# Performance work log

Measured on AMD Instinct MI355X. Metric: run time of the kernel, lower is better.

The kernel has to match this reference:

```python
import jax, jax.numpy as jnp
import numpy as np

B, S, D, H = 2, 2048, 1024, 16
DK = D // H
MAX_REL = 2047          # clip range for relative distances
REL_DIM = 64            # rel_embedding dim, summed over


def setup_inputs() -> dict:
    key = jax.random.key(0)
    ks = jax.random.split(key, 12)
    sc = 1.0 / np.sqrt(D)
    inp = {
        "q": jax.random.normal(ks[0], (B, S, D), jnp.float32),
        "k": jax.random.normal(ks[1], (B, S, D), jnp.float32),
        "v": jax.random.normal(ks[2], (B, S, D), jnp.float32),
        "Wq": jax.random.normal(ks[3], (D, D), jnp.float32) * sc,
        "bq": jnp.zeros((D,), jnp.float32),
        "Wk": jax.random.normal(ks[4], (D, D), jnp.float32) * sc,
        "bk": jnp.zeros((D,), jnp.float32),
        "Wv": jax.random.normal(ks[5], (D, D), jnp.float32) * sc,
        "bv": jnp.zeros((D,), jnp.float32),
        "Wo": jax.random.normal(ks[6], (D, D), jnp.float32) * sc,
        "bo": jnp.zeros((D,), jnp.float32),
        "rel_table": jax.random.normal(ks[7], (2 * MAX_REL + 1, REL_DIM), jnp.float32) * 0.02,
        "mask": jnp.tril(jnp.ones((1, 1, S, S), jnp.bool_)),  # causal
    }
    return inp


def reference(q, k, v, Wq, bq, Wk, bk, Wv, bv, Wo, bo, rel_table, mask):
    def split_heads(x):
        # [B,S,D] -> [B,H,S,DK]
        return x.reshape(B, -1, H, DK).transpose(0, 2, 1, 3)

    Q = split_heads(q @ Wq + bq)
    K = split_heads(k @ Wk + bk)
    V = split_heads(v @ Wv + bv)

    scores = jnp.einsum("bhqd,bhkd->bhqk", Q, K) / jnp.sqrt(jnp.float32(DK))

    # relative position bias: table[clip(j - i)] summed over rel dim -> [S,S]
    rel_idx = jnp.clip(jnp.arange(S)[None, :] - jnp.arange(S)[:, None],
                       -MAX_REL, MAX_REL) + MAX_REL
    rel_bias = rel_table[rel_idx].sum(-1)  # [S,S]
    scores = scores + rel_bias[None, None]

    scores = jnp.where(mask, scores, jnp.float32(-1e20))
    attn = jax.nn.softmax(scores, axis=-1)

    out = jnp.einsum("bhqk,bhkd->bhqd", attn, V)
    out = out.transpose(0, 2, 1, 3).reshape(B, -1, D)
    return out @ Wo + bo
```

## Files before the change

kernel.cpp:

```cpp
#include <hip/hip_runtime.h>

#define SEQ 2048
#define DIM 1024
#define NH 16
#define HD 64
#define NB 2

typedef __bf16 bf16x8 __attribute__((ext_vector_type(8)));
typedef float f32x4 __attribute__((ext_vector_type(4)));
typedef float f32x4v __attribute__((ext_vector_type(4)));
typedef float f32x4u __attribute__((ext_vector_type(4), aligned(4)));
typedef unsigned short us8 __attribute__((ext_vector_type(8)));
typedef unsigned short us4 __attribute__((ext_vector_type(4)));

#define LOG2E 1.44269504f

__device__ __forceinline__ unsigned short bfbits(float f) {
  __bf16 h = (__bf16)f;
  return __builtin_bit_cast(unsigned short, h);
}

__global__ __launch_bounds__(256) void wconv4_kernel(
    const float* __restrict__ W0, const float* __restrict__ W1,
    const float* __restrict__ W2, const float* __restrict__ W3,
    unsigned short* __restrict__ Wt, const float* __restrict__ rel_table,
    float* __restrict__ relsum, const float* __restrict__ Aq,
    const float* __restrict__ Ak, const float* __restrict__ Av,
    unsigned short* __restrict__ Bq, unsigned short* __restrict__ Bk,
    unsigned short* __restrict__ Bv) {
  int z = blockIdx.z;
  int tid = threadIdx.x;
  if (z == 4) {
    int ti = blockIdx.y * 16 + blockIdx.x;
    int i = ti * 256 + tid;
    if (i < 4095) {
      const f32x4v* row = reinterpret_cast<const f32x4v*>(rel_table + (size_t)i * 64);
      float s = 0.f;
      for (int d = 0; d < 16; ++d) {
        f32x4v v = row[d];
        s += v[0] + v[1] + v[2] + v[3];
      }
      relsum[i] = s * LOG2E - 8.0f;
    }
    return;
  }
  if (z >= 5) {
    const float* src = (z == 5) ? Aq : (z == 6) ? Ak : Av;
    unsigned short* dst = (z == 5) ? Bq : (z == 6) ? Bk : Bv;
    int bid2 = blockIdx.y * 16 + blockIdx.x;
    int c0 = bid2 * 256 + tid;
    for (int j = 0; j < 8; ++j) {
      size_t e = ((size_t)(c0 + j * 65536)) * 8;
      f32x4v v0 = *reinterpret_cast<const f32x4v*>(src + e);
      f32x4v v1 = *reinterpret_cast<const f32x4v*>(src + e + 4);
      us8 o;
      o[0] = bfbits(v0[0]); o[1] = bfbits(v0[1]); o[2] = bfbits(v0[2]); o[3] = bfbits(v0[3]);
      o[4] = bfbits(v1[0]); o[5] = bfbits(v1[1]); o[6] = bfbits(v1[2]); o[7] = bfbits(v1[3]);
      *reinterpret_cast<us8*>(dst + e) = o;
    }
    return;
  }
  __shared__ unsigned short T[64][68];
  const float* W = (z == 0) ? W0 : (z == 1) ? W1 : (z == 2) ? W2 : W3;
  unsigned short* out = Wt + (size_t)z * 1024 * 1024;
  int r0 = blockIdx.y * 64;
  int c0 = blockIdx.x * 64;
  for (int it = 0; it < 4; ++it) {
    int s = tid + it * 256;
    int r = s >> 4;
    int c4 = (s & 15) * 4;
    f32x4v v = *reinterpret_cast<const f32x4v*>(W + (size_t)(r0 + r) * 1024 + c0 + c4);
    us4 o;
    o[0] = bfbits(v[0]); o[1] = bfbits(v[1]); o[2] = bfbits(v[2]); o[3] = bfbits(v[3]);
    *reinterpret_cast<us4*>(&T[r][c4]) = o;
  }
  __syncthreads();
  for (int it = 0; it < 2; ++it) {
    int s = tid + it * 256;
    int n = s >> 3;
    int k8 = (s & 7) * 8;
    us8 o;
    for (int e = 0; e < 8; ++e) o[e] = T[k8 + e][n];
    *reinterpret_cast<us8*>(out + (size_t)(c0 + n) * 1024 + r0 + k8) = o;
  }
}

__global__ __launch_bounds__(256) void gemm_qkv_kernel(
    const unsigned short* __restrict__ Aq, const unsigned short* __restrict__ Ak,
    const unsigned short* __restrict__ Av, const unsigned short* __restrict__ WTb,
    const float* __restrict__ bq, const float* __restrict__ bk,
    const float* __restrict__ bv, unsigned short* __restrict__ Qb,
    unsigned short* __restrict__ Kb, unsigned short* __restrict__ Vt,
    float qscale) {
  constexpr int N = 1024, K = 1024;
  int o = (blockIdx.x & 7) * 192 + (blockIdx.x >> 3);
  int z = o >> 9;
  int r2 = o & 511;
  int row0 = (r2 >> 4) * 128;
  int col0 = (r2 & 15) * 64;
  const unsigned short* A = (z == 0) ? Aq : (z == 1) ? Ak : Av;
  const unsigned short* WT = WTb + (size_t)z * N * K;
  const float* bias = (z == 0) ? bq : (z == 1) ? bk : bv;
  float oscale = (z == 0) ? qscale : 1.0f;

  int tid = threadIdx.x;
  int w = tid >> 6;
  int lane = tid & 63;
  int lg = lane >> 4;
  int li = lane & 15;
  int wr = (w >> 1) * 64;
  int wc = (w & 1) * 32;

  __shared__ unsigned short As[2][128][72];
  __shared__ unsigned short Ws[2][64][72];

  us8 ab16[4];
  us8 wreg[2];

#define GLOAD(KS)                                                         \
  {                                                                       \
    int k0 = (KS) * 64;                                                   \
    for (int it = 0; it < 4; ++it) {                                      \
      int s = tid + it * 256;                                             \
      int r = s >> 3;                                                     \
      int cg = (s & 7) * 8;                                               \
      ab16[it] = *reinterpret_cast<const us8*>(                           \
          A + (size_t)(row0 + r) * K + k0 + cg);                          \
    }                                                                     \
    for (int it = 0; it < 2; ++it) {                                      \
      int s = tid + it * 256;                                             \
      int c = s >> 3;                                                     \
      int kg = (s & 7) * 8;                                               \
      wreg[it] = *reinterpret_cast<const us8*>(                           \
          WT + (size_t)(col0 + c) * K + k0 + kg);                         \
    }                                                                     \
  }

#define SWRITE(B)                                                         \
  {                                                                       \
    for (int it = 0; it < 4; ++it) {                                      \
      int s = tid + it * 256;                                             \
      int r = s >> 3;                                                     \
      int cg = (s & 7) * 8;                                               \
      *reinterpret_cast<us8*>(&As[B][r][cg]) = ab16[it];                  \
    }                                                                     \
    for (int it = 0; it < 2; ++it) {                                      \
      int s = tid + it * 256;                                             \
      int c = s >> 3;                                                     \
      int kg = (s & 7) * 8;                                               \
      *reinterpret_cast<us8*>(&Ws[B][c][kg]) = wreg[it];                  \
    }                                                                     \
  }

  f32x4 acc[4][2] = {};

  GLOAD(0);
  SWRITE(0);
  GLOAD(1);
  __syncthreads();

  for (int ks = 0; ks < 16; ++ks) {
    if (ks < 15) SWRITE((ks + 1) & 1);
    if (ks < 14) GLOAD(ks + 2);
    int B = ks & 1;
    for (int kk = 0; kk < 2; ++kk) {
      bf16x8 af[4], bfr[2];
      for (int m = 0; m < 4; ++m)
        af[m] = *reinterpret_cast<const bf16x8*>(&As[B][wr + m * 16 + li][kk * 32 + lg * 8]);
      for (int n = 0; n < 2; ++n)
        bfr[n] = *reinterpret_cast<const bf16x8*>(&Ws[B][wc + n * 16 + li][kk * 32 + lg * 8]);
      for (int m = 0; m < 4; ++m)
        for (int n = 0; n < 2; ++n)
          acc[m][n] = __builtin_amdgcn_mfma_f32_16x16x32_bf16(af[m], bfr[n], acc[m][n], 0, 0, 0);
    }
    __syncthreads();
  }

  for (int m = 0; m < 4; ++m)
    for (int n = 0; n < 2; ++n) {
      int row = row0 + wr + m * 16 + lg * 4;
      int col = col0 + wc + n * 16 + li;
      float v4[4];
      for (int r = 0; r < 4; ++r) v4[r] = (acc[m][n][r] + bias[col]) * oscale;
      if (z == 2) {
        int bb = row >> 11, seq = row & 2047;
        int hh = col >> 6, dk = col & 63;
        us4 o4;
        o4[0] = bfbits(v4[0]); o4[1] = bfbits(v4[1]);
        o4[2] = bfbits(v4[2]); o4[3] = bfbits(v4[3]);
        *reinterpret_cast<us4*>(
            Vt + ((size_t)(bb * NH + hh) * HD + dk) * SEQ + seq) = o4;
      } else {
        unsigned short* Cp = (z == 0) ? Qb : Kb;
        for (int r = 0; r < 4; ++r)
          Cp[(size_t)(row + r) * N + col] = bfbits(v4[r]);
      }
    }
#undef GLOAD
#undef SWRITE
}

__global__ __launch_bounds__(256) void gemm_out_kernel(
    const unsigned short* __restrict__ A, const unsigned short* __restrict__ WT,
    const float* __restrict__ bias, float* __restrict__ Cp) {
  constexpr int N = 1024, K = 1024;
  int o = ((blockIdx.x & 7) << 6) | (blockIdx.x >> 3);
  int col0 = (o & 15) * 64;
  int row0 = (o >> 4) * 128;
  int tid = threadIdx.x;
  int w = tid >> 6;
  int lane = tid & 63;
  int lg = lane >> 4;
  int li = lane & 15;
  int wr = (w >> 1) * 64;
  int wc = (w & 1) * 32;

  __shared__ unsigned short As[2][128][72];
  __shared__ unsigned short Ws[2][64][72];

  us8 ab16[4];
  us8 wreg[2];

#define GLOAD(KS)                                                         \
  {                                                                       \
    int k0 = (KS) * 64;                                                   \
    for (int it = 0; it < 4; ++it) {                                      \
      int s = tid + it * 256;                                             \
      int r = s >> 3;                                                     \
      int cg = (s & 7) * 8;                                               \
      ab16[it] = *reinterpret_cast<const us8*>(                           \
          A + (size_t)(row0 + r) * K + k0 + cg);                          \
    }                                                                     \
    for (int it = 0; it < 2; ++it) {                                      \
      int s = tid + it * 256;                                             \
      int c = s >> 3;                                                     \
      int kg = (s & 7) * 8;                                               \
      wreg[it] = *reinterpret_cast<const us8*>(                           \
          WT + (size_t)(col0 + c) * K + k0 + kg);                         \
    }                                                                     \
  }

#define SWRITE(B)                                                         \
  {                                                                       \
    for (int it = 0; it < 4; ++it) {                                      \
      int s = tid + it * 256;                                             \
      int r = s >> 3;                                                     \
      int cg = (s & 7) * 8;                                               \
      *reinterpret_cast<us8*>(&As[B][r][cg]) = ab16[it];                  \
    }                                                                     \
    for (int it = 0; it < 2; ++it) {                                      \
      int s = tid + it * 256;                                             \
      int c = s >> 3;                                                     \
      int kg = (s & 7) * 8;                                               \
      *reinterpret_cast<us8*>(&Ws[B][c][kg]) = wreg[it];                  \
    }                                                                     \
  }

  f32x4 acc[4][2] = {};

  GLOAD(0);
  SWRITE(0);
  GLOAD(1);
  __syncthreads();

  for (int ks = 0; ks < 16; ++ks) {
    if (ks < 15) SWRITE((ks + 1) & 1);
    if (ks < 14) GLOAD(ks + 2);
    int B = ks & 1;
    for (int kk = 0; kk < 2; ++kk) {
      bf16x8 af[4], bfr[2];
      for (int m = 0; m < 4; ++m)
        af[m] = *reinterpret_cast<const bf16x8*>(&As[B][wr + m * 16 + li][kk * 32 + lg * 8]);
      for (int n = 0; n < 2; ++n)
        bfr[n] = *reinterpret_cast<const bf16x8*>(&Ws[B][wc + n * 16 + li][kk * 32 + lg * 8]);
      for (int m = 0; m < 4; ++m)
        for (int n = 0; n < 2; ++n)
          acc[m][n] = __builtin_amdgcn_mfma_f32_16x16x32_bf16(af[m], bfr[n], acc[m][n], 0, 0, 0);
    }
    __syncthreads();
  }

  for (int m = 0; m < 4; ++m)
    for (int n = 0; n < 2; ++n)
      for (int r = 0; r < 4; ++r) {
        int row = row0 + wr + m * 16 + lg * 4 + r;
        int col = col0 + wc + n * 16 + li;
        Cp[(size_t)row * N + col] = acc[m][n][r] + bias[col];
      }
#undef GLOAD
#undef SWRITE
}

__global__ __launch_bounds__(256) void attn_kernel(
    const unsigned short* __restrict__ Qb, const unsigned short* __restrict__ Kb,
    const unsigned short* __restrict__ Vt, const float* __restrict__ relsum,
    unsigned short* __restrict__ Ob) {
  int r0_ = blockIdx.x >> 3;
  int xcd = blockIdx.x & 7;
  int qt = 31 - (r0_ >> 2);
  int bh = xcd * 4 + (r0_ & 3);
  int h = bh & 15;
  int b = bh >> 4;

  int tid = threadIdx.x;
  int w = tid >> 6;
  int lane = tid & 63;
  int lg = lane >> 4;
  int li = lane & 15;

  __shared__ unsigned short Ks[64][72];
  __shared__ unsigned short VtF[64 * 72];
  __shared__ __bf16 Ps[4][16][72];

  int key0 = tid >> 3;
  int cg0 = (tid & 7) * 8;
  int dk0 = tid >> 3;
  int k8 = (tid & 7) * 8;
  const unsigned short* kptr = Kb + ((size_t)(b * SEQ + key0)) * DIM + h * HD + cg0;
  const unsigned short* vtp = Vt + ((size_t)(b * NH + h) * HD + dk0) * SEQ + k8;

  unsigned vidx0 = ((unsigned)(dk0 * 72 + k8)) ^ ((((unsigned)dk0 >> 3) & 7u) << 3);
  unsigned vidx1 = ((unsigned)((dk0 + 32) * 72 + k8)) ^
                   ((((unsigned)(dk0 + 32) >> 3) & 7u) << 3);

  us8 krg0, krg1, vrg0, vrg1;

#define LOAD_REGS(TT)                                                     \
  {                                                                       \
    size_t koff = (size_t)(TT) * 64 * DIM;                                \
    krg0 = *reinterpret_cast<const us8*>(kptr + koff);                    \
    krg1 = *reinterpret_cast<const us8*>(kptr + koff + 32 * DIM);         \
    vrg0 = *reinterpret_cast<const us8*>(vtp + (TT) * 64);                \
    vrg1 = *reinterpret_cast<const us8*>(vtp + 32 * SEQ + (TT) * 64);     \
  }

#define WRITE_TILE()                                                      \
  {                                                                       \
    *reinterpret_cast<us8*>(&Ks[key0][cg0]) = krg0;                       \
    *reinterpret_cast<us8*>(&Ks[key0 + 32][cg0]) = krg1;                  \
    *reinterpret_cast<us8*>(&VtF[vidx0]) = vrg0;                          \
    *reinterpret_cast<us8*>(&VtF[vidx1]) = vrg1;                          \
  }

  LOAD_REGS(0);

  int qrow = qt * 64 + w * 16 + li;
  const unsigned short* qb = Qb + ((size_t)(b * SEQ + qrow)) * DIM + h * HD;
  bf16x8 qa0 = *reinterpret_cast<const bf16x8*>(qb + lg * 8);
  bf16x8 qa1 = *reinterpret_cast<const bf16x8*>(qb + 32 + lg * 8);

  f32x4 o_acc[4] = {};
  float l_row[4] = {0.f, 0.f, 0.f, 0.f};
  int i0 = qt * 64 + w * 16 + lg * 4;

  for (int t = 0; t <= qt; ++t) {
    __syncthreads();
    WRITE_TILE();
    __syncthreads();

    if (t < qt) LOAD_REGS(t + 1);

    f32x4 s_acc[4] = {};
    __builtin_amdgcn_s_setprio(1);
    for (int kk = 0; kk < 2; ++kk) {
      bf16x8 qa = kk ? qa1 : qa0;
      for (int n = 0; n < 4; ++n) {
        bf16x8 kb = *reinterpret_cast<const bf16x8*>(&Ks[n * 16 + li][kk * 32 + lg * 8]);
        s_acc[n] = __builtin_amdgcn_mfma_f32_16x16x32_bf16(qa, kb, s_acc[n], 0, 0, 0);
      }
    }
    __builtin_amdgcn_s_setprio(0);

    int Cbase = (t - qt) * 64 - (w * 16 + lg * 4) + li + 2047;
    if (t == qt) {
      for (int n = 0; n < 4; ++n) {
        int Cn = Cbase + n * 16;
        f32x4u rel4 = *reinterpret_cast<const f32x4u*>(&relsum[Cn - 3]);
        for (int r = 0; r < 4; ++r) {
          float sv = s_acc[n][r] + rel4[3 - r];
          sv = (Cn - r > 2047) ? -1e30f : sv;
          float e = exp2f(sv);
          s_acc[n][r] = e;
          l_row[r] += e;
        }
      }
    } else {
      for (int n = 0; n < 4; ++n) {
        int Cn = Cbase + n * 16;
        f32x4u rel4 = *reinterpret_cast<const f32x4u*>(&relsum[Cn - 3]);
        for (int r = 0; r < 4; ++r) {
          float e = exp2f(s_acc[n][r] + rel4[3 - r]);
          s_acc[n][r] = e;
          l_row[r] += e;
        }
      }
    }

    for (int n = 0; n < 4; ++n)
      for (int r = 0; r < 4; ++r)
        Ps[w][lg * 4 + r][n * 16 + li] = (__bf16)s_acc[n][r];
    asm volatile("s_waitcnt lgkmcnt(0)" ::: "memory");
    __builtin_amdgcn_sched_barrier(0);

    __builtin_amdgcn_s_setprio(1);
    for (int kk = 0; kk < 2; ++kk) {
      bf16x8 pa = *reinterpret_cast<const bf16x8*>(&Ps[w][li][kk * 32 + lg * 8]);
      for (int n = 0; n < 4; ++n) {
        int dk = n * 16 + li;
        unsigned idx = ((unsigned)(dk * 72 + kk * 32 + lg * 8)) ^
                       ((((unsigned)dk >> 3) & 7u) << 3);
        bf16x8 vb = *reinterpret_cast<const bf16x8*>(&VtF[idx]);
        o_acc[n] = __builtin_amdgcn_mfma_f32_16x16x32_bf16(pa, vb, o_acc[n], 0, 0, 0);
      }
    }
    __builtin_amdgcn_s_setprio(0);
  }

  for (int msk = 1; msk < 16; msk <<= 1)
    for (int r = 0; r < 4; ++r) l_row[r] += __shfl_xor(l_row[r], msk);
  float inv_l[4];
  for (int r = 0; r < 4; ++r) inv_l[r] = 1.f / l_row[r];
  for (int n = 0; n < 4; ++n)
    for (int r = 0; r < 4; ++r) {
      int row = i0 + r;
      int dk = n * 16 + li;
      Ob[((size_t)(b * SEQ + row)) * DIM + h * HD + dk] =
          bfbits(o_acc[n][r] * inv_l[r]);
    }
#undef LOAD_REGS
#undef WRITE_TILE
}

extern "C" void kernel_launch(void* const* d_in, const int* in_sizes, int n_in,
                              void* d_out, int out_size, void* d_ws, size_t ws_size,
                              hipStream_t stream) {
  const float* q = (const float*)d_in[0];
  const float* k = (const float*)d_in[1];
  const float* v = (const float*)d_in[2];
  const float* Wq = (const float*)d_in[3];
  const float* bq = (const float*)d_in[4];
  const float* Wk = (const float*)d_in[5];
  const float* bk = (const float*)d_in[6];
  const float* Wv = (const float*)d_in[7];
  const float* bv = (const float*)d_in[8];
  const float* Wo = (const float*)d_in[9];
  const float* bo = (const float*)d_in[10];
  const float* rel = (const float*)d_in[11];

  char* ws = (char*)d_ws;
  const size_t MATB = (size_t)NB * SEQ * DIM * sizeof(unsigned short);
  const size_t WTE = (size_t)DIM * DIM;
  unsigned short* Qb = (unsigned short*)(ws);
  unsigned short* Kb = (unsigned short*)(ws + MATB);
  unsigned short* Vt = (unsigned short*)(ws + 2 * MATB);
  unsigned short* Ob = (unsigned short*)(ws + 3 * MATB);
  float* relsum = (float*)(ws + 4 * MATB);
  unsigned short* WT = (unsigned short*)(ws + 4 * MATB + 65536);

  unsigned short* Abq = (unsigned short*)d_out;
  unsigned short* Abk = (unsigned short*)d_out + (size_t)NB * SEQ * DIM;
  unsigned short* Abv = Ob;

  wconv4_kernel<<<dim3(16, 16, 8), 256, 0, stream>>>(
      Wq, Wk, Wv, Wo, WT, rel, relsum, q, k, v, Abq, Abk, Abv);

  const float qscale = 0.125f * LOG2E;
  gemm_qkv_kernel<<<dim3(1536), 256, 0, stream>>>(Abq, Abk, Abv, WT, bq, bk, bv,
                                                  Qb, Kb, Vt, qscale);

  attn_kernel<<<dim3(1024), 256, 0, stream>>>(Qb, Kb, Vt, relsum, Ob);

  gemm_out_kernel<<<dim3(512), 256, 0, stream>>>(Ob, WT + 3 * WTE, bo, (float*)d_out);
}
```

Measured before the change: 124.7 us.

## Use direct global-to-LDS loads with XOR-swizzled tiles in projection GEMMs

Replaces the register-staged global load plus LDS store in both projection GEMMs with global_load_lds 16-byte direct copies into a packed 64-wide tile. It drops the padded layout in favour of an XOR swizzle on 16-byte groups to avoid bank conflicts on the MFMA fragment reads. The shared loop body is factored into a macro. The aim is to save VGPRs and issue slots on staging, but the loop now has only one prefetch stage and no explicit wait on the async LDS writes beyond __syncthreads.

```diff
diff --git a/kernel.cpp b/kernel.cpp
--- a/kernel.cpp
+++ b/kernel.cpp
@@ -18,6 +18,12 @@
 __device__ __forceinline__ unsigned short bfbits(float f) {
   __bf16 h = (__bf16)f;
   return __builtin_bit_cast(unsigned short, h);
+}
+
+__device__ __forceinline__ void gload16(const unsigned short* g, unsigned short* l) {
+  __builtin_amdgcn_global_load_lds(
+      (const __attribute__((address_space(1))) unsigned int*)(const void*)g,
+      (__attribute__((address_space(3))) unsigned int*)(void*)l, 16, 0, 0);
 }
 
 __global__ __launch_bounds__(256) void wconv4_kernel(
@@ -85,6 +91,74 @@
   }
 }
 
+#define GEMM_CORE(A_, WT_)                                                   \
+  __shared__ unsigned short As[2][128 * 64];                                 \
+  __shared__ unsigned short Ws[2][64 * 64];                                  \
+  int tid = threadIdx.x;                                                     \
+  int w = tid >> 6;                                                          \
+  int lane = tid & 63;                                                       \
+  int lg = lane >> 4;                                                        \
+  int li = lane & 15;                                                        \
+  int wr = (w >> 1) * 64;                                                    \
+  int wc = (w & 1) * 32;                                                     \
+  int swz = li & 7;                                                          \
+  f32x4 acc[4][2] = {};                                                      \
+        \
+  int sA0 = tid;                                                             \
+  int rA0 = sA0 >> 3, gA0 = (sA0 & 7) ^ (rA0 & 7);                           \
+  int sW0 = tid;                                                             \
+  int rW0 = sW0 >> 3, gW0 = (sW0 & 7) ^ (rW0 & 7);                           \
+  (void)sW0;                                                                 \
+  _Pragma("nounroll")                                                        \
+  for (int dummy = 0; dummy < 1; ++dummy) {}                                 \
+                                    \
+  {                                                                          \
+    for (int it = 0; it < 4; ++it) {                                         \
+      int s = tid + it * 256;                                                \
+      int r = s >> 3, g = (s & 7) ^ (r & 7);                                 \
+      gload16(A_ + (size_t)(row0 + r) * 1024 + g * 8, &As[0][s * 8]);        \
+    }                                                                        \
+    for (int it = 0; it < 2; ++it) {                                         \
+      int s = tid + it * 256;                                                \
+      int r = s >> 3, g = (s & 7) ^ (r & 7);                                 \
+      gload16(WT_ + (size_t)(col0 + r) * 1024 + g * 8, &Ws[0][s * 8]);       \
+    }                                                                        \
+  }                                                                          \
+  __syncthreads();                                                           \
+  for (int ks = 0; ks < 16; ++ks) {                                          \
+    if (ks < 15) {                                                           \
+      int k0 = (ks + 1) * 64;                                                \
+      int B2 = (ks + 1) & 1;                                                 \
+      for (int it = 0; it < 4; ++it) {                                       \
+        int s = tid + it * 256;                                              \
+        int r = s >> 3, g = (s & 7) ^ (r & 7);                               \
+        gload16(A_ + (size_t)(row0 + r) * 1024 + k0 + g * 8, &As[B2][s * 8]);\
+      }                                                                      \
+      for (int it = 0; it < 2; ++it) {                                       \
+        int s = tid + it * 256;                                              \
+        int r = s >> 3, g = (s & 7) ^ (r & 7);                               \
+        gload16(WT_ + (size_t)(col0 + r) * 1024 + k0 + g * 8, &Ws[B2][s * 8]);\
+      }                                                                      \
+    }                                                                        \
+    int B = ks & 1;                                                          \
+    for (int kk = 0; kk < 2; ++kk) {                                         \
+      bf16x8 af[4], bfr[2];                                                  \
+      int gidx = ((kk << 2) | lg) ^ swz;                                     \
+      for (int m = 0; m < 4; ++m)                                            \
+        af[m] = *reinterpret_cast<const bf16x8*>(                            \
+            &As[B][(wr + m * 16 + li) * 64 + gidx * 8]);                     \
+      for (int n = 0; n < 2; ++n)                                            \
+        bfr[n] = *reinterpret_cast<const bf16x8*>(                           \
+            &Ws[B][(wc + n * 16 + li) * 64 + gidx * 8]);                     \
+      for (int m = 0; m < 4; ++m)                                            \
+        for (int n = 0; n < 2; ++n)                                          \
+          acc[m][n] = __builtin_amdgcn_mfma_f32_16x16x32_bf16(               \
+              af[m], bfr[n], acc[m][n], 0, 0, 0);                            \
+    }                                                                        \
+    __syncthreads();                                                         \
+  }                                                                          \
+  (void)rA0; (void)gA0; (void)rW0; (void)gW0; (void)sA0;
+
 __global__ __launch_bounds__(256) void gemm_qkv_kernel(
     const unsigned short* __restrict__ Aq, const unsigned short* __restrict__ Ak,
     const unsigned short* __restrict__ Av, const unsigned short* __restrict__ WTb,
@@ -92,89 +166,17 @@
     const float* __restrict__ bv, unsigned short* __restrict__ Qb,
     unsigned short* __restrict__ Kb, unsigned short* __restrict__ Vt,
     float qscale) {
-  constexpr int N = 1024, K = 1024;
   int o = (blockIdx.x & 7) * 192 + (blockIdx.x >> 3);
   int z = o >> 9;
   int r2 = o & 511;
   int row0 = (r2 >> 4) * 128;
   int col0 = (r2 & 15) * 64;
   const unsigned short* A = (z == 0) ? Aq : (z == 1) ? Ak : Av;
-  const unsigned short* WT = WTb + (size_t)z * N * K;
+  const unsigned short* WT = WTb + (size_t)z * 1024 * 1024;
   const float* bias = (z == 0) ? bq : (z == 1) ? bk : bv;
   float oscale = (z == 0) ? qscale : 1.0f;
 
-  int tid = threadIdx.x;
-  int w = tid >> 6;
-  int lane = tid & 63;
-  int lg = lane >> 4;
-  int li = lane & 15;
-  int wr = (w >> 1) * 64;
-  int wc = (w & 1) * 32;
-
-  __shared__ unsigned short As[2][128][72];
-  __shared__ unsigned short Ws[2][64][72];
-
-  us8 ab16[4];
-  us8 wreg[2];
-
-#define GLOAD(KS)                                                         \
-  {                                                                       \
-    int k0 = (KS) * 64;                                                   \
-    for (int it = 0; it < 4; ++it) {                                      \
-      int s = tid + it * 256;                                             \
-      int r = s >> 3;                                                     \
-      int cg = (s & 7) * 8;                                               \
-      ab16[it] = *reinterpret_cast<const us8*>(                           \
-          A + (size_t)(row0 + r) * K + k0 + cg);                          \
-    }                                                                     \
-    for (int it = 0; it < 2; ++it) {                                      \
-      int s = tid + it * 256;                                             \
-      int c = s >> 3;                                                     \
-      int kg = (s & 7) * 8;                                               \
-      wreg[it] = *reinterpret_cast<const us8*>(                           \
-          WT + (size_t)(col0 + c) * K + k0 + kg);                         \
-    }                                                                     \
-  }
-
-#define SWRITE(B)                                                         \
-  {                                                                       \
-    for (int it = 0; it < 4; ++it) {                                      \
-      int s = tid + it * 256;                                             \
-      int r = s >> 3;                                                     \
-      int cg = (s & 7) * 8;                                               \
-      *reinterpret_cast<us8*>(&As[B][r][cg]) = ab16[it];                  \
-    }                                                                     \
-    for (int it = 0; it < 2; ++it) {                                      \
-      int s = tid + it * 256;                                             \
-      int c = s >> 3;                                                     \
-      int kg = (s & 7) * 8;                                               \
-      *reinterpret_cast<us8*>(&Ws[B][c][kg]) = wreg[it];                  \
-    }                                                                     \
-  }
-
-  f32x4 acc[4][2] = {};
-
-  GLOAD(0);
-  SWRITE(0);
-  GLOAD(1);
-  __syncthreads();
-
-  for (int ks = 0; ks < 16; ++ks) {
-    if (ks < 15) SWRITE((ks + 1) & 1);
-    if (ks < 14) GLOAD(ks + 2);
-    int B = ks & 1;
-    for (int kk = 0; kk < 2; ++kk) {
-      bf16x8 af[4], bfr[2];
-      for (int m = 0; m < 4; ++m)
-        af[m] = *reinterpret_cast<const bf16x8*>(&As[B][wr + m * 16 + li][kk * 32 + lg * 8]);
-      for (int n = 0; n < 2; ++n)
-        bfr[n] = *reinterpret_cast<const bf16x8*>(&Ws[B][wc + n * 16 + li][kk * 32 + lg * 8]);
-      for (int m = 0; m < 4; ++m)
-        for (int n = 0; n < 2; ++n)
-          acc[m][n] = __builtin_amdgcn_mfma_f32_16x16x32_bf16(af[m], bfr[n], acc[m][n], 0, 0, 0);
-    }
-    __syncthreads();
-  }
+  GEMM_CORE(A, WT)
 
   for (int m = 0; m < 4; ++m)
     for (int n = 0; n < 2; ++n) {
@@ -193,102 +195,27 @@
       } else {
         unsigned short* Cp = (z == 0) ? Qb : Kb;
         for (int r = 0; r < 4; ++r)
-          Cp[(size_t)(row + r) * N + col] = bfbits(v4[r]);
-      }
-    }
-#undef GLOAD
-#undef SWRITE
+          Cp[(size_t)(row + r) * 1024 + col] = bfbits(v4[r]);
+      }
+    }
 }
 
 __global__ __launch_bounds__(256) void gemm_out_kernel(
     const unsigned short* __restrict__ A, const unsigned short* __restrict__ WT,
     const float* __restrict__ bias, float* __restrict__ Cp) {
-  constexpr int N = 1024, K = 1024;
   int o = ((blockIdx.x & 7) << 6) | (blockIdx.x >> 3);
   int col0 = (o & 15) * 64;
   int row0 = (o >> 4) * 128;
-  int tid = threadIdx.x;
-  int w = tid >> 6;
-  int lane = tid & 63;
-  int lg = lane >> 4;
-  int li = lane & 15;
-  int wr = (w >> 1) * 64;
-  int wc = (w & 1) * 32;
-
-  __shared__ unsigned short As[2][128][72];
-  __shared__ unsigned short Ws[2][64][72];
-
-  us8 ab16[4];
-  us8 wreg[2];
-
-#define GLOAD(KS)                                                         \
-  {                                                                       \
-    int k0 = (KS) * 64;                                                   \
-    for (int it = 0; it < 4; ++it) {                                      \
-      int s = tid + it * 256;                                             \
-      int r = s >> 3;                                                     \
-      int cg = (s & 7) * 8;                                               \
-      ab16[it] = *reinterpret_cast<const us8*>(                           \
-          A + (size_t)(row0 + r) * K + k0 + cg);                          \
-    }                                                                     \
-    for (int it = 0; it < 2; ++it) {                                      \
-      int s = tid + it * 256;                                             \
-      int c = s >> 3;                                                     \
-      int kg = (s & 7) * 8;                                               \
-      wreg[it] = *reinterpret_cast<const us8*>(                           \
-          WT + (size_t)(col0 + c) * K + k0 + kg);                         \
-    }                                                                     \
-  }
-
-#define SWRITE(B)                                                         \
-  {                                                                       \
-    for (int it = 0; it < 4; ++it) {                                      \
-      int s = tid + it * 256;                                             \
-      int r = s >> 3;                                                     \
-      int cg = (s & 7) * 8;                                               \
-      *reinterpret_cast<us8*>(&As[B][r][cg]) = ab16[it];                  \
-    }                                                                     \
-    for (int it = 0; it < 2; ++it) {                                      \
-      int s = tid + it * 256;                                             \
-      int c = s >> 3;                                                     \
-      int kg = (s & 7) * 8;                                               \
-      *reinterpret_cast<us8*>(&Ws[B][c][kg]) = wreg[it];                  \
-    }                                                                     \
-  }
-
-  f32x4 acc[4][2] = {};
-
-  GLOAD(0);
-  SWRITE(0);
-  GLOAD(1);
-  __syncthreads();
-
-  for (int ks = 0; ks < 16; ++ks) {
-    if (ks < 15) SWRITE((ks + 1) & 1);
-    if (ks < 14) GLOAD(ks + 2);
-    int B = ks & 1;
-    for (int kk = 0; kk < 2; ++kk) {
-      bf16x8 af[4], bfr[2];
-      for (int m = 0; m < 4; ++m)
-        af[m] = *reinterpret_cast<const bf16x8*>(&As[B][wr + m * 16 + li][kk * 32 + lg * 8]);
-      for (int n = 0; n < 2; ++n)
-        bfr[n] = *reinterpret_cast<const bf16x8*>(&Ws[B][wc + n * 16 + li][kk * 32 + lg * 8]);
-      for (int m = 0; m < 4; ++m)
-        for (int n = 0; n < 2; ++n)
-          acc[m][n] = __builtin_amdgcn_mfma_f32_16x16x32_bf16(af[m], bfr[n], acc[m][n], 0, 0, 0);
-    }
-    __syncthreads();
-  }
+
+  GEMM_CORE(A, WT)
 
   for (int m = 0; m < 4; ++m)
     for (int n = 0; n < 2; ++n)
       for (int r = 0; r < 4; ++r) {
         int row = row0 + wr + m * 16 + lg * 4 + r;
         int col = col0 + wc + n * 16 + li;
-        Cp[(size_t)row * N + col] = acc[m][n][r] + bias[col];
-      }
-#undef GLOAD
-#undef SWRITE
+        Cp[(size_t)row * 1024 + col] = acc[m][n][r] + bias[col];
+      }
 }
 
 __global__ __launch_bounds__(256) void attn_kernel(
```

Result: faster. 120.9 us (-3.0%).
